# Performance work log

Measured on AMD Instinct MI355X. Metric: run time of the kernel, lower is better.

## Reference

```python
import jax, jax.numpy as jnp
import numpy as np

N_DRUG, E_DRUG, F_DRUG = 50000, 1000000, 256
N_DIS, E_DIS, F_DIS = 20000, 640000, 128
NHID2 = 64


def setup_inputs() -> dict:
    key = jax.random.key(0)
    k = jax.random.split(key, 8)
    drug_x = jax.random.normal(k[0], (N_DRUG, F_DRUG), dtype=jnp.float32)
    drug_edge_index = jax.random.randint(k[1], (2, E_DRUG), 0, N_DRUG, dtype=jnp.int64)
    dis_x = jax.random.normal(k[2], (N_DIS, F_DIS), dtype=jnp.float32)
    dis_edge_index = jax.random.randint(k[3], (2, E_DIS), 0, N_DIS, dtype=jnp.int64)
    # GCNConv weights (glorot-ish scale) and biases for the single layer of each GCN
    W1 = jax.random.normal(k[4], (F_DRUG, NHID2), dtype=jnp.float32) / np.sqrt(F_DRUG)
    b1 = jnp.zeros((NHID2,), dtype=jnp.float32)
    W2 = jax.random.normal(k[5], (F_DIS, NHID2), dtype=jnp.float32) / np.sqrt(F_DIS)
    b2 = jnp.zeros((NHID2,), dtype=jnp.float32)
    return {
        "drug_x": drug_x, "dis_x": dis_x,
        "W1": W1, "b1": b1, "W2": W2, "b2": b2,
        "drug_edge_index": drug_edge_index, "dis_edge_index": dis_edge_index,
    }


def _gcn_conv(x, edge_index, W, b, num_nodes):
    # GCNConv with normalize=False: out[i] = sum_{j in N(i)} (x @ W)[j] + b
    h = x @ W                       # [N, nhid2]
    src, dst = edge_index[0], edge_index[1]
    msg = h[src]                    # [E, nhid2] gather
    agg = jax.ops.segment_sum(msg, dst, num_segments=num_nodes)  # scatter-add
    return agg + b


def reference(drug_x, dis_x, W1, b1, W2, b2, drug_edge_index, dis_edge_index):
    emb1 = _gcn_conv(drug_x, drug_edge_index, W1, b1, N_DRUG)
    emb2 = _gcn_conv(dis_x, dis_edge_index, W2, b2, N_DIS)
    return (emb1, emb2)
```

## Files before the change

kernel.cpp:

```cpp
#include <hip/hip_runtime.h>

#define N_DRUG 50000
#define F_DRUG 256
#define E_DRUG 1000000
#define N_DIS  20000
#define F_DIS  128
#define E_DIS  640000
#define NHID   64

#define NBKT  512
#define SH1   7
#define ROWS1 128
#define NBB1  391
#define CAPB1 3072
#define SH2   6
#define ROWS2 64
#define NBB2  313
#define CAPB2 2560

#define BINCH 4096
#define NCH1  245
#define NCH2  157

#define NBG1  391
#define NBG2  157

typedef __bf16 bf16x8 __attribute__((ext_vector_type(8)));
typedef float  f32x4  __attribute__((ext_vector_type(4)));

__device__ inline float bfl(unsigned u) {
    union { unsigned i; float f; } c; c.i = u << 16; return c.f;
}
__device__ inline float bfh(unsigned u) {
    union { unsigned i; float f; } c; c.i = u & 0xffff0000u; return c.f;
}

__global__ void zero_kernel(int* __restrict__ g1, int* __restrict__ g2) {
    for (int i = threadIdx.x; i < NBB1; i += 256) g1[i] = 0;
    for (int i = threadIdx.x; i < NBB2; i += 256) g2[i] = 0;
}

__global__ void __launch_bounds__(256)
phase1_kernel(const int* __restrict__ ei1, int* __restrict__ gcur1, unsigned* __restrict__ bin1,
              const int* __restrict__ ei2, int* __restrict__ gcur2, unsigned* __restrict__ bin2,
              const float* __restrict__ x1, const float* __restrict__ W1, __bf16* __restrict__ h1,
              const float* __restrict__ x2, const float* __restrict__ W2, __bf16* __restrict__ h2) {
    __shared__ int smem[8192];
    const int bid = blockIdx.x;
    const int tid = threadIdx.x;

    if (bid < NCH1 + NCH2) {
        const int* ei; int* gcur; unsigned* binned; int E, shift, capb, cb;
        if (bid < NCH1) {
            ei = ei1; gcur = gcur1; binned = bin1; E = E_DRUG; shift = SH1; capb = CAPB1; cb = bid;
        } else {
            ei = ei2; gcur = gcur2; binned = bin2; E = E_DIS; shift = SH2; capb = CAPB2; cb = bid - NCH1;
        }
        int* hist  = smem;
        int* excl  = smem + 512;
        int* gbase = smem + 1024;
        int* buf   = smem + 1536;

        const int base = cb * BINCH;
        const int total = min(BINCH, E - base);

        for (int i = tid; i < NBKT; i += 256) hist[i] = 0;
        __syncthreads();

        unsigned my[16]; int mybkt[16]; int myloc[16];
#pragma unroll
        for (int j = 0; j < 16; ++j) {
            int e = base + j * 256 + tid;
            if (e < E) {
                int s = ei[e];
                int d = ei[E + e];
                my[j] = ((unsigned)s << 16) | (unsigned)d;
                mybkt[j] = d >> shift;
                myloc[j] = atomicAdd(&hist[mybkt[j]], 1);
            } else {
                mybkt[j] = -1;
            }
        }
        __syncthreads();

        if (tid < 64) {
            int run = 0;
            for (int ch = 0; ch < NBKT / 64; ++ch) {
                int v = hist[ch * 64 + tid];
                int incl = v;
#pragma unroll
                for (int off = 1; off < 64; off <<= 1) {
                    int t = __shfl_up(incl, off);
                    if (tid >= off) incl += t;
                }
                excl[ch * 64 + tid] = run + incl - v;
                run += __shfl(incl, 63);
            }
        }
        __syncthreads();

        for (int i = tid; i < NBKT; i += 256) {
            int c = hist[i];
            if (c) gbase[i] = atomicAdd(&gcur[i], c);
        }
        __syncthreads();

#pragma unroll
        for (int j = 0; j < 16; ++j)
            if (mybkt[j] >= 0) buf[excl[mybkt[j]] + myloc[j]] = (int)my[j];
        __syncthreads();

        for (int s = tid; s < total; s += 256) {
            unsigned p = (unsigned)buf[s];
            int b = (int)(p & 0xFFFFu) >> shift;
            int idx = gbase[b] + (s - excl[b]);
            if (idx < capb)
                binned[(size_t)b * capb + idx] = p;
        }
    } else {
        __bf16* Wlds = (__bf16*)smem;
        const float* x; const float* W; __bf16* h; int M, K, lb;
        int gb = bid - (NCH1 + NCH2);
        if (gb < NBG1) {
            x = x1; W = W1; h = h1; M = N_DRUG; K = F_DRUG; lb = gb;
        } else {
            x = x2; W = W2; h = h2; M = N_DIS; K = F_DIS; lb = gb - NBG1;
        }

        for (int idx = tid; idx < K * 64; idx += 256) {
            int k = idx >> 6, col = idx & 63;
            Wlds[((k >> 3) * 64 + col) * 8 + (k & 7)] = (__bf16)W[idx];
        }
        __syncthreads();

        const int wid = tid >> 6, lane = tid & 63;
        const int l15 = lane & 15, lhi = lane >> 4;
        const int r0 = lb * 128 + wid * 32;
        if (r0 >= M) return;

        f32x4 acc[2][4];
#pragma unroll
        for (int m = 0; m < 2; ++m)
#pragma unroll
            for (int c = 0; c < 4; ++c) acc[m][c] = {0.f, 0.f, 0.f, 0.f};

        int rowA0 = r0 + l15;
        int rowA1 = r0 + 16 + l15;
        int cr0 = rowA0 < M ? rowA0 : M - 1;
        int cr1 = rowA1 < M ? rowA1 : M - 1;
        const float* pA0 = x + (size_t)cr0 * K + lhi * 8;
        const float* pA1 = x + (size_t)cr1 * K + lhi * 8;
        const bf16x8* Wv = (const bf16x8*)Wlds;

        for (int kk = 0; kk < K; kk += 32) {
            float4 a0l = *(const float4*)(pA0 + kk);
            float4 a0h = *(const float4*)(pA0 + kk + 4);
            float4 a1l = *(const float4*)(pA1 + kk);
            float4 a1h = *(const float4*)(pA1 + kk + 4);
            bf16x8 af0, af1;
            af0[0] = (__bf16)a0l.x; af0[1] = (__bf16)a0l.y;
            af0[2] = (__bf16)a0l.z; af0[3] = (__bf16)a0l.w;
            af0[4] = (__bf16)a0h.x; af0[5] = (__bf16)a0h.y;
            af0[6] = (__bf16)a0h.z; af0[7] = (__bf16)a0h.w;
            af1[0] = (__bf16)a1l.x; af1[1] = (__bf16)a1l.y;
            af1[2] = (__bf16)a1l.z; af1[3] = (__bf16)a1l.w;
            af1[4] = (__bf16)a1h.x; af1[5] = (__bf16)a1h.y;
            af1[6] = (__bf16)a1h.z; af1[7] = (__bf16)a1h.w;
            const int kblk = (kk >> 3) + lhi;
#pragma unroll
            for (int c = 0; c < 4; ++c) {
                bf16x8 bf = Wv[kblk * 64 + c * 16 + l15];
                acc[0][c] = __builtin_amdgcn_mfma_f32_16x16x32_bf16(af0, bf, acc[0][c], 0, 0, 0);
                acc[1][c] = __builtin_amdgcn_mfma_f32_16x16x32_bf16(af1, bf, acc[1][c], 0, 0, 0);
            }
        }

#pragma unroll
        for (int m = 0; m < 2; ++m) {
            int rbase = r0 + m * 16 + lhi * 4;
#pragma unroll
            for (int c = 0; c < 4; ++c) {
                int col = c * 16 + l15;
#pragma unroll
                for (int r = 0; r < 4; ++r) {
                    int row = rbase + r;
                    if (row < M) h[(size_t)row * 64 + col] = (__bf16)acc[m][c][r];
                }
            }
        }
    }
}

__global__ void __launch_bounds__(512)
sortgather_kernel(const unsigned* __restrict__ bin1, const int* __restrict__ gc1,
                  const unsigned short* __restrict__ h1, const float* __restrict__ bias1,
                  float* __restrict__ out1,
                  const unsigned* __restrict__ bin2, const int* __restrict__ gc2,
                  const unsigned short* __restrict__ h2, const float* __restrict__ bias2,
                  float* __restrict__ out2) {
    __shared__ int hist[ROWS1];
    __shared__ int nstart[ROWS1 + 1];
    __shared__ int cur[ROWS1];
    __shared__ int srcbuf[CAPB1];

    const unsigned* pb; const unsigned short* hbf; const float* bias; float* out;
    int N, b, rows, capb, cnt;
    if ((int)blockIdx.x < NBB1) {
        b = blockIdx.x;
        pb = bin1 + (size_t)b * CAPB1; hbf = h1; bias = bias1; out = out1;
        N = N_DRUG; rows = ROWS1; capb = CAPB1;
        cnt = gc1[b];
    } else {
        b = blockIdx.x - NBB1;
        pb = bin2 + (size_t)b * CAPB2; hbf = h2; bias = bias2; out = out2;
        N = N_DIS; rows = ROWS2; capb = CAPB2;
        cnt = gc2[b];
    }
    cnt = min(cnt, capb);

    const int tid = threadIdx.x;
    const int lane = tid & 63, w = tid >> 6;
    const int mask = rows - 1;

    for (int i = tid; i < rows; i += 512) hist[i] = 0;
    __syncthreads();

    unsigned pv[6];
#pragma unroll
    for (int j = 0; j < 6; ++j) {
        int i = j * 512 + tid;
        pv[j] = (i < cnt) ? pb[i] : 0xFFFFFFFFu;
    }

#pragma unroll
    for (int j = 0; j < 6; ++j)
        if (pv[j] != 0xFFFFFFFFu) atomicAdd(&hist[(int)(pv[j] & (unsigned)mask)], 1);
    __syncthreads();

    if (tid < 64) {
        int run = 0;
        for (int ch = 0; ch * 64 < rows; ++ch) {
            int v = hist[ch * 64 + tid];
            int incl = v;
#pragma unroll
            for (int off = 1; off < 64; off <<= 1) {
                int t = __shfl_up(incl, off);
                if (tid >= off) incl += t;
            }
            nstart[ch * 64 + tid] = run + incl - v;
            run += __shfl(incl, 63);
        }
        if (tid == 0) nstart[rows] = run;
    }
    __syncthreads();
    for (int i = tid; i < rows; i += 512) cur[i] = nstart[i];
    __syncthreads();

#pragma unroll
    for (int j = 0; j < 6; ++j)
        if (pv[j] != 0xFFFFFFFFu) {
            int pos = atomicAdd(&cur[(int)(pv[j] & (unsigned)mask)], 1);
            srcbuf[pos] = (int)(pv[j] >> 16);
        }
    __syncthreads();

    const int q = lane & 15, g = lane >> 4;
    const float4 bv = *(const float4*)(bias + (q << 2));
    const int rowbase = b * rows;
    for (int n = w; n < rows; n += 8) {
        int row = rowbase + n;
        int j0 = nstart[n], j1 = nstart[n + 1];
        float ax0 = 0.f, ay0 = 0.f, az0 = 0.f, aw0 = 0.f;
        float ax1 = 0.f, ay1 = 0.f, az1 = 0.f, aw1 = 0.f;
        int j = j0 + g;
        for (; j + 4 < j1; j += 8) {
            int s0 = srcbuf[j];
            int s1 = srcbuf[j + 4];
            uint2 u0 = *(const uint2*)(hbf + ((size_t)s0 << 6) + (q << 2));
            uint2 u1 = *(const uint2*)(hbf + ((size_t)s1 << 6) + (q << 2));
            ax0 += bfl(u0.x); ay0 += bfh(u0.x); az0 += bfl(u0.y); aw0 += bfh(u0.y);
            ax1 += bfl(u1.x); ay1 += bfh(u1.x); az1 += bfl(u1.y); aw1 += bfh(u1.y);
        }
        if (j < j1) {
            int s0 = srcbuf[j];
            uint2 u0 = *(const uint2*)(hbf + ((size_t)s0 << 6) + (q << 2));
            ax0 += bfl(u0.x); ay0 += bfh(u0.x); az0 += bfl(u0.y); aw0 += bfh(u0.y);
        }
        float fx = ax0 + ax1, fy = ay0 + ay1, fz = az0 + az1, fw = aw0 + aw1;
        fx += __shfl_xor(fx, 16); fy += __shfl_xor(fy, 16);
        fz += __shfl_xor(fz, 16); fw += __shfl_xor(fw, 16);
        fx += __shfl_xor(fx, 32); fy += __shfl_xor(fy, 32);
        fz += __shfl_xor(fz, 32); fw += __shfl_xor(fw, 32);
        if (g == 0 && row < N) {
            float4 o = make_float4(fx + bv.x, fy + bv.y, fz + bv.z, fw + bv.w);
            *(float4*)(out + (size_t)row * 64 + (q << 2)) = o;
        }
    }
}

extern "C" void kernel_launch(void* const* d_in, const int* in_sizes, int n_in,
                              void* d_out, int out_size, void* d_ws, size_t ws_size,
                              hipStream_t stream) {
    const float* drug_x = (const float*)d_in[0];
    const float* dis_x  = (const float*)d_in[1];
    const float* W1     = (const float*)d_in[2];
    const float* b1     = (const float*)d_in[3];
    const float* W2     = (const float*)d_in[4];
    const float* b2     = (const float*)d_in[5];
    const int*   ei1    = (const int*)d_in[6];
    const int*   ei2    = (const int*)d_in[7];
    float* out = (float*)d_out;

    char* p = (char*)d_ws;
    __bf16* h1 = (__bf16*)p;    p += (size_t)N_DRUG * NHID * 2;
    __bf16* h2 = (__bf16*)p;    p += (size_t)N_DIS  * NHID * 2;
    int* gcur1 = (int*)p;       p += ((NBB1 + 3) & ~3) * 4;
    int* gcur2 = (int*)p;       p += ((NBB2 + 3) & ~3) * 4;
    unsigned* bin1 = (unsigned*)p;  p += (size_t)NBB1 * CAPB1 * 4;
    unsigned* bin2 = (unsigned*)p;

    zero_kernel<<<1, 256, 0, stream>>>(gcur1, gcur2);
    phase1_kernel<<<NCH1 + NCH2 + NBG1 + NBG2, 256, 0, stream>>>(
        ei1, gcur1, bin1, ei2, gcur2, bin2,
        drug_x, W1, h1, dis_x, W2, h2);
    sortgather_kernel<<<NBB1 + NBB2, 512, 0, stream>>>(
        bin1, gcur1, (const unsigned short*)h1, b1, out,
        bin2, gcur2, (const unsigned short*)h2, b2, out + (size_t)N_DRUG * NHID);
}
```

Baseline: 64.99 us.

## Widen gather loads to 16B, permute block order, replace zero kernel with memset

```diff
diff --git a/kernel.cpp b/kernel.cpp
--- a/kernel.cpp
+++ b/kernel.cpp
@@ -25,6 +25,9 @@
 #define NBG1  391
 #define NBG2  157
 
+#define NP1   950
+#define NP2   704
+
 typedef __bf16 bf16x8 __attribute__((ext_vector_type(8)));
 typedef float  f32x4  __attribute__((ext_vector_type(4)));
 
@@ -33,11 +36,6 @@
 }
 __device__ inline float bfh(unsigned u) {
     union { unsigned i; float f; } c; c.i = u & 0xffff0000u; return c.f;
-}
-
-__global__ void zero_kernel(int* __restrict__ g1, int* __restrict__ g2) {
-    for (int i = threadIdx.x; i < NBB1; i += 256) g1[i] = 0;
-    for (int i = threadIdx.x; i < NBB2; i += 256) g2[i] = 0;
 }
 
 __global__ void __launch_bounds__(256)
@@ -46,7 +44,7 @@
               const float* __restrict__ x1, const float* __restrict__ W1, __bf16* __restrict__ h1,
               const float* __restrict__ x2, const float* __restrict__ W2, __bf16* __restrict__ h2) {
     __shared__ int smem[8192];
-    const int bid = blockIdx.x;
+    const int bid = (int)(((long long)blockIdx.x * 401) % NP1);
     const int tid = threadIdx.x;
 
     if (bid < NCH1 + NCH2) {
@@ -203,15 +201,17 @@
     __shared__ int cur[ROWS1];
     __shared__ int srcbuf[CAPB1];
 
+    const int bm = (int)(((long long)blockIdx.x * 313) % NP2);
+
     const unsigned* pb; const unsigned short* hbf; const float* bias; float* out;
     int N, b, rows, capb, cnt;
-    if ((int)blockIdx.x < NBB1) {
-        b = blockIdx.x;
+    if (bm < NBB1) {
+        b = bm;
         pb = bin1 + (size_t)b * CAPB1; hbf = h1; bias = bias1; out = out1;
         N = N_DRUG; rows = ROWS1; capb = CAPB1;
         cnt = gc1[b];
     } else {
-        b = blockIdx.x - NBB1;
+        b = bm - NBB1;
         pb = bin2 + (size_t)b * CAPB2; hbf = h2; bias = bias2; out = out2;
         N = N_DIS; rows = ROWS2; capb = CAPB2;
         cnt = gc2[b];
@@ -264,36 +264,48 @@
         }
     __syncthreads();
 
-    const int q = lane & 15, g = lane >> 4;
-    const float4 bv = *(const float4*)(bias + (q << 2));
+    const int q = lane & 7, g = lane >> 3;
+    const float4 bva = *(const float4*)(bias + (q << 3));
+    const float4 bvb = *(const float4*)(bias + (q << 3) + 4);
     const int rowbase = b * rows;
     for (int n = w; n < rows; n += 8) {
         int row = rowbase + n;
         int j0 = nstart[n], j1 = nstart[n + 1];
-        float ax0 = 0.f, ay0 = 0.f, az0 = 0.f, aw0 = 0.f;
-        float ax1 = 0.f, ay1 = 0.f, az1 = 0.f, aw1 = 0.f;
+        float a0 = 0.f, a1 = 0.f, a2 = 0.f, a3 = 0.f;
+        float a4 = 0.f, a5 = 0.f, a6 = 0.f, a7 = 0.f;
+        float c0 = 0.f, c1 = 0.f, c2 = 0.f, c3 = 0.f;
+        float c4 = 0.f, c5 = 0.f, c6 = 0.f, c7 = 0.f;
         int j = j0 + g;
-        for (; j + 4 < j1; j += 8) {
+        for (; j + 8 < j1; j += 16) {
             int s0 = srcbuf[j];
-            int s1 = srcbuf[j + 4];
-            uint2 u0 = *(const uint2*)(hbf + ((size_t)s0 << 6) + (q << 2));
-            uint2 u1 = *(const uint2*)(hbf + ((size_t)s1 << 6) + (q << 2));
-            ax0 += bfl(u0.x); ay0 += bfh(u0.x); az0 += bfl(u0.y); aw0 += bfh(u0.y);
-            ax1 += bfl(u1.x); ay1 += bfh(u1.x); az1 += bfl(u1.y); aw1 += bfh(u1.y);
+            int s1 = srcbuf[j + 8];
+            uint4 u0 = *(const uint4*)(hbf + ((size_t)s0 << 6) + (q << 3));
+            uint4 u1 = *(const uint4*)(hbf + ((size_t)s1 << 6) + (q << 3));
+            a0 += bfl(u0.x); a1 += bfh(u0.x); a2 += bfl(u0.y); a3 += bfh(u0.y);
+            a4 += bfl(u0.z); a5 += bfh(u0.z); a6 += bfl(u0.w); a7 += bfh(u0.w);
+            c0 += bfl(u1.x); c1 += bfh(u1.x); c2 += bfl(u1.y); c3 += bfh(u1.y);
+            c4 += bfl(u1.z); c5 += bfh(u1.z); c6 += bfl(u1.w); c7 += bfh(u1.w);
         }
         if (j < j1) {
             int s0 = srcbuf[j];
-            uint2 u0 = *(const uint2*)(hbf + ((size_t)s0 << 6) + (q << 2));
-            ax0 += bfl(u0.x); ay0 += bfh(u0.x); az0 += bfl(u0.y); aw0 += bfh(u0.y);
-        }
-        float fx = ax0 + ax1, fy = ay0 + ay1, fz = az0 + az1, fw = aw0 + aw1;
-        fx += __shfl_xor(fx, 16); fy += __shfl_xor(fy, 16);
-        fz += __shfl_xor(fz, 16); fw += __shfl_xor(fw, 16);
-        fx += __shfl_xor(fx, 32); fy += __shfl_xor(fy, 32);
-        fz += __shfl_xor(fz, 32); fw += __shfl_xor(fw, 32);
+            uint4 u0 = *(const uint4*)(hbf + ((size_t)s0 << 6) + (q << 3));
+            a0 += bfl(u0.x); a1 += bfh(u0.x); a2 += bfl(u0.y); a3 += bfh(u0.y);
+            a4 += bfl(u0.z); a5 += bfh(u0.z); a6 += bfl(u0.w); a7 += bfh(u0.w);
+        }
+        a0 += c0; a1 += c1; a2 += c2; a3 += c3;
+        a4 += c4; a5 += c5; a6 += c6; a7 += c7;
+#pragma unroll
+        for (int off = 8; off < 64; off <<= 1) {
+            a0 += __shfl_xor(a0, off); a1 += __shfl_xor(a1, off);
+            a2 += __shfl_xor(a2, off); a3 += __shfl_xor(a3, off);
+            a4 += __shfl_xor(a4, off); a5 += __shfl_xor(a5, off);
+            a6 += __shfl_xor(a6, off); a7 += __shfl_xor(a7, off);
+        }
         if (g == 0 && row < N) {
-            float4 o = make_float4(fx + bv.x, fy + bv.y, fz + bv.z, fw + bv.w);
-            *(float4*)(out + (size_t)row * 64 + (q << 2)) = o;
+            float4 o1 = make_float4(a0 + bva.x, a1 + bva.y, a2 + bva.z, a3 + bva.w);
+            float4 o2 = make_float4(a4 + bvb.x, a5 + bvb.y, a6 + bvb.z, a7 + bvb.w);
+            *(float4*)(out + (size_t)row * 64 + (q << 3)) = o1;
+            *(float4*)(out + (size_t)row * 64 + (q << 3) + 4) = o2;
         }
     }
 }
@@ -314,16 +326,16 @@
     char* p = (char*)d_ws;
     __bf16* h1 = (__bf16*)p;    p += (size_t)N_DRUG * NHID * 2;
     __bf16* h2 = (__bf16*)p;    p += (size_t)N_DIS  * NHID * 2;
-    int* gcur1 = (int*)p;       p += ((NBB1 + 3) & ~3) * 4;
-    int* gcur2 = (int*)p;       p += ((NBB2 + 3) & ~3) * 4;
+    int* gcur1 = (int*)p;       p += 392 * 4;
+    int* gcur2 = (int*)p;       p += 316 * 4;
     unsigned* bin1 = (unsigned*)p;  p += (size_t)NBB1 * CAPB1 * 4;
     unsigned* bin2 = (unsigned*)p;
 
-    zero_kernel<<<1, 256, 0, stream>>>(gcur1, gcur2);
-    phase1_kernel<<<NCH1 + NCH2 + NBG1 + NBG2, 256, 0, stream>>>(
+    hipMemsetAsync(gcur1, 0, (392 + 316) * sizeof(int), stream);
+    phase1_kernel<<<NP1, 256, 0, stream>>>(
         ei1, gcur1, bin1, ei2, gcur2, bin2,
         drug_x, W1, h1, dis_x, W2, h2);
-    sortgather_kernel<<<NBB1 + NBB2, 512, 0, stream>>>(
+    sortgather_kernel<<<NP2, 512, 0, stream>>>(
         bin1, gcur1, (const unsigned short*)h1, b1, out,
         bin2, gcur2, (const unsigned short*)h2, b2, out + (size_t)N_DRUG * NHID);
 }
```

New measurement: 73.75 us. 13.5% more time.
